# Kernel optimization log

Hardware: AMD Instinct MI355X
Metric: run time of the kernel (lower is better)

The kernel has to match this reference:

```python
import jax, jax.numpy as jnp
import numpy as np

B, NQ, K = 256, 16, 200           # batch, num_neg+1, num_keys
KEY_SIZE, QUERY_SIZE, HIDDEN = 64, 64, 128
NEG_INF_SCALE = -1000000000.0


def setup_inputs() -> dict:
    key = jax.random.key(0)
    ks = jax.random.split(key, 9)
    queries = jax.random.normal(ks[0], (B, NQ, QUERY_SIZE), dtype=jnp.float32)
    keys = jax.random.normal(ks[1], (B, K, KEY_SIZE), dtype=jnp.float32)
    cum_subs_masks = (jax.random.uniform(ks[2], (B, NQ, K, 1)) < 0.3).astype(jnp.float32)
    s = 1.0 / np.sqrt(HIDDEN)
    Wq = jax.random.normal(ks[3], (QUERY_SIZE, HIDDEN), dtype=jnp.float32) * s
    bq = jnp.zeros((HIDDEN,), dtype=jnp.float32)
    Wk = jax.random.normal(ks[4], (KEY_SIZE, HIDDEN), dtype=jnp.float32) * s
    bk = jnp.zeros((HIDDEN,), dtype=jnp.float32)
    Wv = jax.random.normal(ks[5], (HIDDEN, 1), dtype=jnp.float32) * s
    bv = jnp.zeros((1,), dtype=jnp.float32)
    return {"queries": queries, "keys": keys, "cum_subs_masks": cum_subs_masks,
            "num_neg": NQ - 1, "Wq": Wq, "bq": bq, "Wk": Wk, "bk": bk,
            "Wv": Wv, "bv": bv}


def reference(queries, keys, cum_subs_masks, num_neg, Wq, bq, Wk, bk, Wv, bv):
    # project once, broadcast instead of expanding keys per query (same math)
    qh = queries @ Wq + bq                 # (B, NQ, H)
    kh = keys @ Wk + bk                    # (B, K, H)
    h = jnp.tanh(qh[:, :, None, :] + kh[:, None, :, :])   # (B, NQ, K, H)
    scores = h @ Wv + bv                   # (B, NQ, K, 1)
    if cum_subs_masks is not None:
        scores = scores + cum_subs_masks * NEG_INF_SCALE
    attn_weight = jax.nn.softmax(scores, axis=-2)          # softmax over keys
    attn_out = jnp.sum(attn_weight * keys[:, None, :, :], axis=-2)  # (B, NQ, key_size)
    return (attn_out, attn_weight)
```

## Files before the change

kernel.cpp:

```cpp
#include <hip/hip_runtime.h>

namespace {

typedef __attribute__((ext_vector_type(8))) short short8;
typedef __attribute__((ext_vector_type(4))) float f32x4;

constexpr int kNB = 256;
constexpr int kNQ = 16;
constexpr int kNK = 200;
constexpr int kDK = 64;
constexpr int kNH = 128;
constexpr int kThreads = 1024;
constexpr int kS = 132;
constexpr float kNeg = -1000000000.0f;
constexpr float kC2 = 2.8853900817779268f;

constexpr int kKhFloats = kNK * kS;
constexpr int kScFloats = kNQ * kNK;
constexpr int kQhFloats = kNQ * kNH;
constexpr size_t kSmemBytes =
    (size_t)(kKhFloats + kScFloats + kQhFloats) * sizeof(float);

__device__ __forceinline__ float exp2_hw(float x) {
#if defined(__has_builtin)
# if __has_builtin(__builtin_amdgcn_exp2f)
  return __builtin_amdgcn_exp2f(x);
# else
  return __expf(x * 0.69314718055994531f);
# endif
#else
  return __expf(x * 0.69314718055994531f);
#endif
}

template <int CTRL>
__device__ __forceinline__ float dpp_add(float v) {
  int sw = __builtin_amdgcn_update_dpp(0, __float_as_int(v), CTRL, 0xF, 0xF, true);
  return v + __int_as_float(sw);
}

__device__ __forceinline__ short bf_hi(float x) {
  unsigned u = __float_as_uint(x);
  return (short)((u + 0x7FFFu + ((u >> 16) & 1u)) >> 16);
}
__device__ __forceinline__ float bf_f(short s) {
  return __uint_as_float(((unsigned)(unsigned short)s) << 16);
}
__device__ __forceinline__ void split8(float4 a, float4 b, short8& hi, short8& lo) {
  float v[8] = {a.x, a.y, a.z, a.w, b.x, b.y, b.z, b.w};
#pragma unroll
  for (int j = 0; j < 8; ++j) {
    const short h = bf_hi(v[j]);
    hi[j] = h;
    lo[j] = bf_hi(v[j] - bf_f(h));
  }
}

__launch_bounds__(kThreads)
__attribute__((amdgpu_waves_per_eu(4, 4)))
__global__ void bahdanau_fused(const float* __restrict__ queries,
                               const float* __restrict__ keys,
                               const float* __restrict__ masks,
                               const float* __restrict__ Wq,
                               const float* __restrict__ bq,
                               const float* __restrict__ Wk,
                               const float* __restrict__ bk,
                               const float* __restrict__ Wv,
                               float* __restrict__ out_attn,
                               float* __restrict__ out_w) {
  extern __shared__ __align__(16) float smem[];
  float* skh = smem;
  float* ssc = smem + kKhFloats;
  float* sqh = smem + kKhFloats + kScFloats;

  const int tid  = threadIdx.x;
  const int b    = blockIdx.x;
  const int lane = tid & 63;
  const int wave = __builtin_amdgcn_readfirstlane(tid >> 6);
  const int l15  = lane & 15;
  const int q16  = lane >> 4;
  const int hbase = 8 * l15;

  const float* kb = keys + (size_t)b * kNK * kDK;
  const float* qb = queries + (size_t)b * kNQ * kDK;

  {
    const int tc  = wave >> 1;
    const int odd = wave & 1;
    const int col = tc * 16 + l15;
    const int kj0 = q16 * 8;

    short8 bh[2], bl[2];
#pragma unroll
    for (int p = 0; p < 2; ++p) {
      float4 v0, v1;
      v0.x = Wk[(p * 32 + kj0 + 0) * kNH + col];
      v0.y = Wk[(p * 32 + kj0 + 1) * kNH + col];
      v0.z = Wk[(p * 32 + kj0 + 2) * kNH + col];
      v0.w = Wk[(p * 32 + kj0 + 3) * kNH + col];
      v1.x = Wk[(p * 32 + kj0 + 4) * kNH + col];
      v1.y = Wk[(p * 32 + kj0 + 5) * kNH + col];
      v1.z = Wk[(p * 32 + kj0 + 6) * kNH + col];
      v1.w = Wk[(p * 32 + kj0 + 7) * kNH + col];
      split8(v0, v1, bh[p], bl[p]);
    }
    const float bkc = bk[col];

    const int trB = odd ? 7 : 0;
    const int trE = odd ? 13 : 7;
    for (int tr = trB; tr < trE; ++tr) {
      f32x4 acc = {0.f, 0.f, 0.f, 0.f};
      const int row = tr * 16 + l15;
      const bool ok = row < kNK;
#pragma unroll
      for (int p = 0; p < 2; ++p) {
        float4 a0 = {0.f, 0.f, 0.f, 0.f}, a1 = {0.f, 0.f, 0.f, 0.f};
        if (ok) {
          const float* ap = kb + (size_t)row * kDK + p * 32 + kj0;
          a0 = *reinterpret_cast<const float4*>(ap);
          a1 = *reinterpret_cast<const float4*>(ap + 4);
        }
        short8 ah, al;
        split8(a0, a1, ah, al);
        acc = __builtin_amdgcn_mfma_f32_16x16x32_bf16(al, bh[p], acc, 0, 0, 0);
        acc = __builtin_amdgcn_mfma_f32_16x16x32_bf16(ah, bl[p], acc, 0, 0, 0);
        acc = __builtin_amdgcn_mfma_f32_16x16x32_bf16(ah, bh[p], acc, 0, 0, 0);
      }
#pragma unroll
      for (int r = 0; r < 4; ++r) {
        const int rr = tr * 16 + q16 * 4 + r;
        if (rr < kNK) skh[(size_t)rr * kS + col] = exp2_hw(kC2 * (acc[r] + bkc));
      }
    }

    if (odd) {
      short8 qbh[2], qbl[2];
#pragma unroll
      for (int p = 0; p < 2; ++p) {
        float4 v0, v1;
        v0.x = Wq[(p * 32 + kj0 + 0) * kNH + col];
        v0.y = Wq[(p * 32 + kj0 + 1) * kNH + col];
        v0.z = Wq[(p * 32 + kj0 + 2) * kNH + col];
        v0.w = Wq[(p * 32 + kj0 + 3) * kNH + col];
        v1.x = Wq[(p * 32 + kj0 + 4) * kNH + col];
        v1.y = Wq[(p * 32 + kj0 + 5) * kNH + col];
        v1.z = Wq[(p * 32 + kj0 + 6) * kNH + col];
        v1.w = Wq[(p * 32 + kj0 + 7) * kNH + col];
        split8(v0, v1, qbh[p], qbl[p]);
      }
      const float bqc = bq[col];
      f32x4 acc = {0.f, 0.f, 0.f, 0.f};
#pragma unroll
      for (int p = 0; p < 2; ++p) {
        const float* ap = qb + (size_t)l15 * kDK + p * 32 + kj0;
        const float4 a0 = *reinterpret_cast<const float4*>(ap);
        const float4 a1 = *reinterpret_cast<const float4*>(ap + 4);
        short8 ah, al;
        split8(a0, a1, ah, al);
        acc = __builtin_amdgcn_mfma_f32_16x16x32_bf16(al, qbh[p], acc, 0, 0, 0);
        acc = __builtin_amdgcn_mfma_f32_16x16x32_bf16(ah, qbl[p], acc, 0, 0, 0);
        acc = __builtin_amdgcn_mfma_f32_16x16x32_bf16(ah, qbh[p], acc, 0, 0, 0);
      }
#pragma unroll
      for (int r = 0; r < 4; ++r)
        sqh[(size_t)(q16 * 4 + r) * kNH + col] = exp2_hw(kC2 * (acc[r] + bqc));
    }
  }

  float wv2[8];
  {
    const float4 wva = *reinterpret_cast<const float4*>(&Wv[hbase]);
    const float4 wvb = *reinterpret_cast<const float4*>(&Wv[hbase + 4]);
    wv2[0] = -2.0f * wva.x; wv2[1] = -2.0f * wva.y;
    wv2[2] = -2.0f * wva.z; wv2[3] = -2.0f * wva.w;
    wv2[4] = -2.0f * wvb.x; wv2[5] = -2.0f * wvb.y;
    wv2[6] = -2.0f * wvb.z; wv2[7] = -2.0f * wvb.w;
  }

  __syncthreads();

  const int qg = wave >> 2;
  const int kg = wave & 3;
  float qreg[4][8];
#pragma unroll
  for (int qi = 0; qi < 4; ++qi) {
    const float4 qa  = *reinterpret_cast<const float4*>(&sqh[(4 * qg + qi) * kNH + hbase]);
    const float4 qb4 = *reinterpret_cast<const float4*>(&sqh[(4 * qg + qi) * kNH + hbase + 4]);
    qreg[qi][0] = qa.x;  qreg[qi][1] = qa.y;  qreg[qi][2] = qa.z;  qreg[qi][3] = qa.w;
    qreg[qi][4] = qb4.x; qreg[qi][5] = qb4.y; qreg[qi][6] = qb4.z; qreg[qi][7] = qb4.w;
  }
#pragma unroll
  for (int qi = 0; qi < 4; ++qi)
#pragma unroll
    for (int m = 0; m < 8; ++m) asm volatile("" : "+v"(qreg[qi][m]));

  {
    auto score_k = [&](int k) {
      const float* krow = &skh[(size_t)k * kS + hbase];
      const float4 ka  = *reinterpret_cast<const float4*>(krow);
      const float4 kb4 = *reinterpret_cast<const float4*>(krow + 4);
#pragma unroll
      for (int qi = 0; qi < 4; ++qi) {
        const float e0 = qreg[qi][0] * ka.x;
        const float e1 = qreg[qi][1] * ka.y;
        const float e2 = qreg[qi][2] * ka.z;
        const float e3 = qreg[qi][3] * ka.w;
        const float e4 = qreg[qi][4] * kb4.x;
        const float e5 = qreg[qi][5] * kb4.y;
        const float e6 = qreg[qi][6] * kb4.z;
        const float e7 = qreg[qi][7] * kb4.w;
        const float r0 = __builtin_amdgcn_rcpf(1.0f + e0);
        const float r1 = __builtin_amdgcn_rcpf(1.0f + e1);
        const float r2 = __builtin_amdgcn_rcpf(1.0f + e2);
        const float r3 = __builtin_amdgcn_rcpf(1.0f + e3);
        const float r4 = __builtin_amdgcn_rcpf(1.0f + e4);
        const float r5 = __builtin_amdgcn_rcpf(1.0f + e5);
        const float r6 = __builtin_amdgcn_rcpf(1.0f + e6);
        const float r7 = __builtin_amdgcn_rcpf(1.0f + e7);
        float acc0 = wv2[0] * r0;
        acc0 = fmaf(wv2[1], r1, acc0);
        acc0 = fmaf(wv2[2], r2, acc0);
        acc0 = fmaf(wv2[3], r3, acc0);
        float acc1 = wv2[4] * r4;
        acc1 = fmaf(wv2[5], r5, acc1);
        acc1 = fmaf(wv2[6], r6, acc1);
        acc1 = fmaf(wv2[7], r7, acc1);
        float acc = acc0 + acc1;
        acc = dpp_add<0xB1>(acc);
        acc = dpp_add<0x4E>(acc);
        acc = dpp_add<0x141>(acc);
        acc = dpp_add<0x140>(acc);
        if (l15 == 0) ssc[(4 * qg + qi) * kNK + k] = acc;
      }
    };
    for (int i = 0; i < 12; ++i) score_k(16 * i + 4 * kg + q16);
    if (kg < 2) score_k(192 + 4 * kg + q16);
  }

  const float* mrow = masks + ((size_t)b * kNQ + wave) * kNK;
  const bool tail = lane < (kNK - 192);
  const float mm0 = mrow[lane];
  const float mm1 = mrow[lane + 64];
  const float mm2 = mrow[lane + 128];
  const float mm3 = tail ? mrow[lane + 192] : 0.0f;

  __syncthreads();

  {
    const float* sr = &ssc[wave * kNK];
    float v0 = fmaf(mm0, kNeg, sr[lane]);
    float v1 = fmaf(mm1, kNeg, sr[lane + 64]);
    float v2 = fmaf(mm2, kNeg, sr[lane + 128]);
    float v3 = tail ? fmaf(mm3, kNeg, sr[lane + 192]) : -1e30f;
    float m = fmaxf(fmaxf(v0, v1), fmaxf(v2, v3));
#pragma unroll
    for (int off = 32; off > 0; off >>= 1) m = fmaxf(m, __shfl_xor(m, off, 64));
    const float e0 = __expf(v0 - m);
    const float e1 = __expf(v1 - m);
    const float e2 = __expf(v2 - m);
    const float e3 = tail ? __expf(v3 - m) : 0.f;
    float sum = (e0 + e1) + (e2 + e3);
#pragma unroll
    for (int off = 32; off > 0; off >>= 1) sum += __shfl_xor(sum, off, 64);
    const float rs = __builtin_amdgcn_rcpf(sum);
    float* og = out_w + ((size_t)b * kNQ + wave) * kNK;
    float* sw = &ssc[wave * kNK];
    const float w0 = e0 * rs, w1 = e1 * rs, w2 = e2 * rs, w3 = e3 * rs;
    sw[lane]       = w0;  og[lane]       = w0;
    sw[lane + 64]  = w1;  og[lane + 64]  = w1;
    sw[lane + 128] = w2;  og[lane + 128] = w2;
    if (tail) { sw[lane + 192] = w3; og[lane + 192] = w3; }
  }
  __syncthreads();

  {
    float* pk = skh;
    const int kstart = 52 * kg;
    const int kend = (kg == 3) ? kNK : (kstart + 52);
    const float* kb2 = kb + lane;
    float acc[4] = {0.f, 0.f, 0.f, 0.f};
    for (int k0 = kstart; k0 < kend; k0 += 4) {
      const float kv0 = kb2[(size_t)(k0 + 0) * kDK];
      const float kv1 = kb2[(size_t)(k0 + 1) * kDK];
      const float kv2 = kb2[(size_t)(k0 + 2) * kDK];
      const float kv3 = kb2[(size_t)(k0 + 3) * kDK];
#pragma unroll
      for (int qi = 0; qi < 4; ++qi) {
        const float4 wq = *reinterpret_cast<const float4*>(&ssc[(4 * qg + qi) * kNK + k0]);
        acc[qi] = fmaf(wq.x, kv0, acc[qi]);
        acc[qi] = fmaf(wq.y, kv1, acc[qi]);
        acc[qi] = fmaf(wq.z, kv2, acc[qi]);
        acc[qi] = fmaf(wq.w, kv3, acc[qi]);
      }
    }
#pragma unroll
    for (int qi = 0; qi < 4; ++qi)
      pk[((4 * qg + qi) * 4 + kg) * kDK + lane] = acc[qi];
  }
  __syncthreads();

  {
    const float* pk = skh;
    const float r = pk[(wave * 4 + 0) * kDK + lane] + pk[(wave * 4 + 1) * kDK + lane] +
                    pk[(wave * 4 + 2) * kDK + lane] + pk[(wave * 4 + 3) * kDK + lane];
    out_attn[((size_t)b * kNQ + wave) * kDK + lane] = r;
  }
}

}

extern "C" void kernel_launch(void* const* d_in, const int* in_sizes, int n_in,
                              void* d_out, int out_size, void* d_ws, size_t ws_size,
                              hipStream_t stream) {
  const float* queries = (const float*)d_in[0];
  const float* keys    = (const float*)d_in[1];
  const float* masks   = (const float*)d_in[2];
  const float* Wq = (const float*)d_in[4];
  const float* bq = (const float*)d_in[5];
  const float* Wk = (const float*)d_in[6];
  const float* bk = (const float*)d_in[7];
  const float* Wv = (const float*)d_in[8];

  float* out_attn = (float*)d_out;
  float* out_w    = out_attn + (size_t)kNB * kNQ * kDK;

  hipFuncSetAttribute((const void*)bahdanau_fused,
                      hipFuncAttributeMaxDynamicSharedMemorySize, (int)kSmemBytes);

  bahdanau_fused<<<kNB, kThreads, kSmemBytes, stream>>>(queries, keys, masks, Wq, bq,
                                                        Wk, bk, Wv, out_attn, out_w);
}
```

Before: 38.40 us.

## Split fused kernel into hidden-half score kernel plus softmax/GEMV kernel

Splits the single fused per-batch kernel into two launches. The first computes projections and partial tanh scores for half of the hidden dimension per block, giving 512 blocks with smaller shared memory, and writes partial scores to workspace. The second sums the two partials, applies mask and softmax, and does the weighted key sum. The aim is more parallelism and occupancy than 256 large blocks offer, at the cost of an extra launch, a workspace round trip, and recomputing the query projection in both halves. It falls back to the fused kernel if the workspace is too small.

Measured after the change: 45.87 us. +19.4%, slower.

```diff
diff --git a/kernel.cpp b/kernel.cpp
--- a/kernel.cpp
+++ b/kernel.cpp
@@ -10,16 +10,11 @@
 constexpr int kNK = 200;
 constexpr int kDK = 64;
 constexpr int kNH = 128;
-constexpr int kThreads = 1024;
-constexpr int kS = 132;
 constexpr float kNeg = -1000000000.0f;
 constexpr float kC2 = 2.8853900817779268f;
 
-constexpr int kKhFloats = kNK * kS;
-constexpr int kScFloats = kNQ * kNK;
-constexpr int kQhFloats = kNQ * kNH;
-constexpr size_t kSmemBytes =
-    (size_t)(kKhFloats + kScFloats + kQhFloats) * sizeof(float);
+constexpr int kS1 = 66;
+constexpr size_t kWsNeed = (size_t)kNB * 2 * kNQ * kNK * sizeof(float);
 
 __device__ __forceinline__ float exp2_hw(float x) {
 #if defined(__has_builtin)
@@ -55,6 +50,252 @@
     lo[j] = bf_hi(v[j] - bf_f(h));
   }
 }
+
+__launch_bounds__(512)
+__attribute__((amdgpu_waves_per_eu(4, 4)))
+__global__ void proj_score(const float* __restrict__ queries,
+                           const float* __restrict__ keys,
+                           const float* __restrict__ Wq,
+                           const float* __restrict__ bq,
+                           const float* __restrict__ Wk,
+                           const float* __restrict__ bk,
+                           const float* __restrict__ Wv,
+                           float* __restrict__ ps) {
+  __shared__ float skh[kNK * kS1];
+  __shared__ float sqh[kNQ * kS1];
+
+  const int tid  = threadIdx.x;
+  const int b    = blockIdx.x >> 1;
+  const int hb   = blockIdx.x & 1;
+  const int lane = tid & 63;
+  const int wave = __builtin_amdgcn_readfirstlane(tid >> 6);
+  const int l15  = lane & 15;
+  const int q16  = lane >> 4;
+
+  const float* kb = keys + (size_t)b * kNK * kDK;
+  const float* qb = queries + (size_t)b * kNQ * kDK;
+
+  {
+    const int tc   = wave >> 1;
+    const int odd  = wave & 1;
+    const int lcol = tc * 16 + l15;
+    const int gcol = hb * 64 + lcol;
+    const int kj0  = q16 * 8;
+
+    short8 bh[2], bl[2];
+#pragma unroll
+    for (int p = 0; p < 2; ++p) {
+      float4 v0, v1;
+      v0.x = Wk[(p * 32 + kj0 + 0) * kNH + gcol];
+      v0.y = Wk[(p * 32 + kj0 + 1) * kNH + gcol];
+      v0.z = Wk[(p * 32 + kj0 + 2) * kNH + gcol];
+      v0.w = Wk[(p * 32 + kj0 + 3) * kNH + gcol];
+      v1.x = Wk[(p * 32 + kj0 + 4) * kNH + gcol];
+      v1.y = Wk[(p * 32 + kj0 + 5) * kNH + gcol];
+      v1.z = Wk[(p * 32 + kj0 + 6) * kNH + gcol];
+      v1.w = Wk[(p * 32 + kj0 + 7) * kNH + gcol];
+      split8(v0, v1, bh[p], bl[p]);
+    }
+    const float bkc = bk[gcol];
+
+    const int trB = odd ? 7 : 0;
+    const int trE = odd ? 13 : 7;
+    for (int tr = trB; tr < trE; ++tr) {
+      f32x4 acc = {0.f, 0.f, 0.f, 0.f};
+      const int row = tr * 16 + l15;
+      const bool ok = row < kNK;
+#pragma unroll
+      for (int p = 0; p < 2; ++p) {
+        float4 a0 = {0.f, 0.f, 0.f, 0.f}, a1 = {0.f, 0.f, 0.f, 0.f};
+        if (ok) {
+          const float* ap = kb + (size_t)row * kDK + p * 32 + kj0;
+          a0 = *reinterpret_cast<const float4*>(ap);
+          a1 = *reinterpret_cast<const float4*>(ap + 4);
+        }
+        short8 ah, al;
+        split8(a0, a1, ah, al);
+        acc = __builtin_amdgcn_mfma_f32_16x16x32_bf16(al, bh[p], acc, 0, 0, 0);
+        acc = __builtin_amdgcn_mfma_f32_16x16x32_bf16(ah, bl[p], acc, 0, 0, 0);
+        acc = __builtin_amdgcn_mfma_f32_16x16x32_bf16(ah, bh[p], acc, 0, 0, 0);
+      }
+#pragma unroll
+      for (int r = 0; r < 4; ++r) {
+        const int rr = tr * 16 + q16 * 4 + r;
+        if (rr < kNK) skh[rr * kS1 + lcol] = exp2_hw(kC2 * (acc[r] + bkc));
+      }
+    }
+
+    if (odd) {
+      short8 qbh[2], qbl[2];
+#pragma unroll
+      for (int p = 0; p < 2; ++p) {
+        float4 v0, v1;
+        v0.x = Wq[(p * 32 + kj0 + 0) * kNH + gcol];
+        v0.y = Wq[(p * 32 + kj0 + 1) * kNH + gcol];
+        v0.z = Wq[(p * 32 + kj0 + 2) * kNH + gcol];
+        v0.w = Wq[(p * 32 + kj0 + 3) * kNH + gcol];
+        v1.x = Wq[(p * 32 + kj0 + 4) * kNH + gcol];
+        v1.y = Wq[(p * 32 + kj0 + 5) * kNH + gcol];
+        v1.z = Wq[(p * 32 + kj0 + 6) * kNH + gcol];
+        v1.w = Wq[(p * 32 + kj0 + 7) * kNH + gcol];
+        split8(v0, v1, qbh[p], qbl[p]);
+      }
+      const float bqc = bq[gcol];
+      f32x4 acc = {0.f, 0.f, 0.f, 0.f};
+#pragma unroll
+      for (int p = 0; p < 2; ++p) {
+        const float* ap = qb + (size_t)l15 * kDK + p * 32 + kj0;
+        const float4 a0 = *reinterpret_cast<const float4*>(ap);
+        const float4 a1 = *reinterpret_cast<const float4*>(ap + 4);
+        short8 ah, al;
+        split8(a0, a1, ah, al);
+        acc = __builtin_amdgcn_mfma_f32_16x16x32_bf16(al, qbh[p], acc, 0, 0, 0);
+        acc = __builtin_amdgcn_mfma_f32_16x16x32_bf16(ah, qbl[p], acc, 0, 0, 0);
+        acc = __builtin_amdgcn_mfma_f32_16x16x32_bf16(ah, qbh[p], acc, 0, 0, 0);
+      }
+#pragma unroll
+      for (int r = 0; r < 4; ++r)
+        sqh[(q16 * 4 + r) * kS1 + lcol] = exp2_hw(kC2 * (acc[r] + bqc));
+    }
+  }
+
+  float wv2[4];
+  {
+    const float4 w4 = *reinterpret_cast<const float4*>(&Wv[hb * 64 + 4 * l15]);
+    wv2[0] = -2.0f * w4.x; wv2[1] = -2.0f * w4.y;
+    wv2[2] = -2.0f * w4.z; wv2[3] = -2.0f * w4.w;
+  }
+
+  __syncthreads();
+
+  const int qg = wave >> 1;
+  const int kg = wave & 1;
+  float qreg[4][4];
+#pragma unroll
+  for (int qi = 0; qi < 4; ++qi) {
+    const float4 q4 = *reinterpret_cast<const float4*>(&sqh[(4 * qg + qi) * kS1 + 4 * l15]);
+    qreg[qi][0] = q4.x; qreg[qi][1] = q4.y; qreg[qi][2] = q4.z; qreg[qi][3] = q4.w;
+  }
+#pragma unroll
+  for (int qi = 0; qi < 4; ++qi)
+#pragma unroll
+    for (int m = 0; m < 4; ++m) asm volatile("" : "+v"(qreg[qi][m]));
+
+  float* pw = ps + ((size_t)(b * 2 + hb) * kNQ) * kNK;
+  for (int i = 0; i < 25; ++i) {
+    const int k = 8 * i + 4 * kg + q16;
+    const float4 ek = *reinterpret_cast<const float4*>(&skh[k * kS1 + 4 * l15]);
+#pragma unroll
+    for (int qi = 0; qi < 4; ++qi) {
+      const float e0 = qreg[qi][0] * ek.x;
+      const float e1 = qreg[qi][1] * ek.y;
+      const float e2 = qreg[qi][2] * ek.z;
+      const float e3 = qreg[qi][3] * ek.w;
+      const float r0 = __builtin_amdgcn_rcpf(1.0f + e0);
+      const float r1 = __builtin_amdgcn_rcpf(1.0f + e1);
+      const float r2 = __builtin_amdgcn_rcpf(1.0f + e2);
+      const float r3 = __builtin_amdgcn_rcpf(1.0f + e3);
+      float acc = wv2[0] * r0;
+      acc = fmaf(wv2[1], r1, acc);
+      acc = fmaf(wv2[2], r2, acc);
+      acc = fmaf(wv2[3], r3, acc);
+      acc = dpp_add<0xB1>(acc);
+      acc = dpp_add<0x4E>(acc);
+      acc = dpp_add<0x141>(acc);
+      acc = dpp_add<0x140>(acc);
+      if (l15 == 0) pw[(4 * qg + qi) * kNK + k] = acc;
+    }
+  }
+}
+
+__launch_bounds__(1024)
+__global__ void softmax_gemv(const float* __restrict__ keys,
+                             const float* __restrict__ masks,
+                             const float* __restrict__ ps,
+                             float* __restrict__ out_attn,
+                             float* __restrict__ out_w) {
+  __shared__ float sw[kNQ * kNK];
+  __shared__ float pk[kNQ * 4 * kDK];
+
+  const int tid  = threadIdx.x;
+  const int b    = blockIdx.x;
+  const int lane = tid & 63;
+  const int wave = __builtin_amdgcn_readfirstlane(tid >> 6);
+
+  const float* kb = keys + (size_t)b * kNK * kDK;
+
+  {
+    const float* p0 = ps + ((size_t)(b * 2 + 0) * kNQ + wave) * kNK;
+    const float* p1 = ps + ((size_t)(b * 2 + 1) * kNQ + wave) * kNK;
+    const float* mrow = masks + ((size_t)b * kNQ + wave) * kNK;
+    const bool tail = lane < (kNK - 192);
+    float v0 = fmaf(mrow[lane],       kNeg, p0[lane]       + p1[lane]);
+    float v1 = fmaf(mrow[lane + 64],  kNeg, p0[lane + 64]  + p1[lane + 64]);
+    float v2 = fmaf(mrow[lane + 128], kNeg, p0[lane + 128] + p1[lane + 128]);
+    float v3 = tail ? fmaf(mrow[lane + 192], kNeg, p0[lane + 192] + p1[lane + 192])
+                    : -1e30f;
+    float m = fmaxf(fmaxf(v0, v1), fmaxf(v2, v3));
+#pragma unroll
+    for (int off = 32; off > 0; off >>= 1) m = fmaxf(m, __shfl_xor(m, off, 64));
+    const float e0 = __expf(v0 - m);
+    const float e1 = __expf(v1 - m);
+    const float e2 = __expf(v2 - m);
+    const float e3 = tail ? __expf(v3 - m) : 0.f;
+    float sum = (e0 + e1) + (e2 + e3);
+#pragma unroll
+    for (int off = 32; off > 0; off >>= 1) sum += __shfl_xor(sum, off, 64);
+    const float rs = __builtin_amdgcn_rcpf(sum);
+    float* og = out_w + ((size_t)b * kNQ + wave) * kNK;
+    float* swr = &sw[wave * kNK];
+    const float w0 = e0 * rs, w1 = e1 * rs, w2 = e2 * rs, w3 = e3 * rs;
+    swr[lane]       = w0;  og[lane]       = w0;
+    swr[lane + 64]  = w1;  og[lane + 64]  = w1;
+    swr[lane + 128] = w2;  og[lane + 128] = w2;
+    if (tail) { swr[lane + 192] = w3; og[lane + 192] = w3; }
+  }
+  __syncthreads();
+
+  {
+    const int qg = wave >> 2;
+    const int kg = wave & 3;
+    const int kstart = 52 * kg;
+    const int kend = (kg == 3) ? kNK : (kstart + 52);
+    const float* kb2 = kb + lane;
+    float acc[4] = {0.f, 0.f, 0.f, 0.f};
+    for (int k0 = kstart; k0 < kend; k0 += 4) {
+      const float kv0 = kb2[(size_t)(k0 + 0) * kDK];
+      const float kv1 = kb2[(size_t)(k0 + 1) * kDK];
+      const float kv2 = kb2[(size_t)(k0 + 2) * kDK];
+      const float kv3 = kb2[(size_t)(k0 + 3) * kDK];
+#pragma unroll
+      for (int qi = 0; qi < 4; ++qi) {
+        const float4 wq = *reinterpret_cast<const float4*>(&sw[(4 * qg + qi) * kNK + k0]);
+        acc[qi] = fmaf(wq.x, kv0, acc[qi]);
+        acc[qi] = fmaf(wq.y, kv1, acc[qi]);
+        acc[qi] = fmaf(wq.z, kv2, acc[qi]);
+        acc[qi] = fmaf(wq.w, kv3, acc[qi]);
+      }
+    }
+#pragma unroll
+    for (int qi = 0; qi < 4; ++qi)
+      pk[((4 * qg + qi) * 4 + kg) * kDK + lane] = acc[qi];
+  }
+  __syncthreads();
+
+  {
+    const float r = pk[(wave * 4 + 0) * kDK + lane] + pk[(wave * 4 + 1) * kDK + lane] +
+                    pk[(wave * 4 + 2) * kDK + lane] + pk[(wave * 4 + 3) * kDK + lane];
+    out_attn[((size_t)b * kNQ + wave) * kDK + lane] = r;
+  }
+}
+
+constexpr int kThreads = 1024;
+constexpr int kS = 132;
+constexpr int kKhFloats = kNK * kS;
+constexpr int kScFloats = kNQ * kNK;
+constexpr int kQhFloats = kNQ * kNH;
+constexpr size_t kSmemBytes =
+    (size_t)(kKhFloats + kScFloats + kQhFloats) * sizeof(float);
 
 __launch_bounds__(kThreads)
 __attribute__((amdgpu_waves_per_eu(4, 4)))
@@ -105,7 +346,6 @@
       split8(v0, v1, bh[p], bl[p]);
     }
     const float bkc = bk[col];
-
     const int trB = odd ? 7 : 0;
     const int trE = odd ? 13 : 7;
     for (int tr = trB; tr < trE; ++tr) {
@@ -132,7 +372,6 @@
         if (rr < kNK) skh[(size_t)rr * kS + col] = exp2_hw(kC2 * (acc[r] + bkc));
       }
     }
-
     if (odd) {
       short8 qbh[2], qbl[2];
 #pragma unroll
@@ -189,10 +428,6 @@
     qreg[qi][0] = qa.x;  qreg[qi][1] = qa.y;  qreg[qi][2] = qa.z;  qreg[qi][3] = qa.w;
     qreg[qi][4] = qb4.x; qreg[qi][5] = qb4.y; qreg[qi][6] = qb4.z; qreg[qi][7] = qb4.w;
   }
-#pragma unroll
-  for (int qi = 0; qi < 4; ++qi)
-#pragma unroll
-    for (int m = 0; m < 8; ++m) asm volatile("" : "+v"(qreg[qi][m]));
 
   {
     auto score_k = [&](int k) {
@@ -264,12 +499,12 @@
     for (int off = 32; off > 0; off >>= 1) sum += __shfl_xor(sum, off, 64);
     const float rs = __builtin_amdgcn_rcpf(sum);
     float* og = out_w + ((size_t)b * kNQ + wave) * kNK;
-    float* sw = &ssc[wave * kNK];
+    float* swr = &ssc[wave * kNK];
     const float w0 = e0 * rs, w1 = e1 * rs, w2 = e2 * rs, w3 = e3 * rs;
-    sw[lane]       = w0;  og[lane]       = w0;
-    sw[lane + 64]  = w1;  og[lane + 64]  = w1;
-    sw[lane + 128] = w2;  og[lane + 128] = w2;
-    if (tail) { sw[lane + 192] = w3; og[lane + 192] = w3; }
+    swr[lane]       = w0;  og[lane]       = w0;
+    swr[lane + 64]  = w1;  og[lane + 64]  = w1;
+    swr[lane + 128] = w2;  og[lane + 128] = w2;
+    if (tail) { swr[lane + 192] = w3; og[lane + 192] = w3; }
   }
   __syncthreads();
 
@@ -324,9 +559,14 @@
   float* out_attn = (float*)d_out;
   float* out_w    = out_attn + (size_t)kNB * kNQ * kDK;
 
-  hipFuncSetAttribute((const void*)bahdanau_fused,
-                      hipFuncAttributeMaxDynamicSharedMemorySize, (int)kSmemBytes);
-
-  bahdanau_fused<<<kNB, kThreads, kSmemBytes, stream>>>(queries, keys, masks, Wq, bq,
-                                                        Wk, bk, Wv, out_attn, out_w);
-}
+  if (ws_size >= kWsNeed) {
+    float* ps = (float*)d_ws;
+    proj_score<<<kNB * 2, 512, 0, stream>>>(queries, keys, Wq, bq, Wk, bk, Wv, ps);
+    softmax_gemv<<<kNB, 1024, 0, stream>>>(keys, masks, ps, out_attn, out_w);
+  } else {
+    hipFuncSetAttribute((const void*)bahdanau_fused,
+                        hipFuncAttributeMaxDynamicSharedMemorySize, (int)kSmemBytes);
+    bahdanau_fused<<<kNB, kThreads, kSmemBytes, stream>>>(queries, keys, masks, Wq, bq,
+                                                          Wk, bk, Wv, out_attn, out_w);
+  }
+}
```

## Halve block to 8 waves and redistribute projection, score and softmax work

Applied to the files above, without the earlier changes.

The block shrinks from 16 to 8 waves, and each stage's work split is redone. Every wave now computes one 16-column slice of both the query and key projections. The score loop is split into 2 key groups instead of 4 and prefetches the next key row from shared memory. Each wave also handles two softmax rows, and the weighted sum reduces 2 partials instead of 4. The bf16 split uses the library conversions and the tanh argument is fused into an fma. The aim is to cut barrier and wave overhead and raise per-wave ILP, at the cost of less parallelism per block.

Result: slower. 39.20 us (+2.1%).

```diff
diff --git a/kernel.cpp b/kernel.cpp
--- a/kernel.cpp
+++ b/kernel.cpp
@@ -1,4 +1,5 @@
 #include <hip/hip_runtime.h>
+#include <hip/hip_bf16.h>
 
 namespace {
 
@@ -10,7 +11,7 @@
 constexpr int kNK = 200;
 constexpr int kDK = 64;
 constexpr int kNH = 128;
-constexpr int kThreads = 1024;
+constexpr int kThreads = 512;
 constexpr int kS = 132;
 constexpr float kNeg = -1000000000.0f;
 constexpr float kC2 = 2.8853900817779268f;
@@ -39,35 +40,29 @@
   return v + __int_as_float(sw);
 }
 
-__device__ __forceinline__ short bf_hi(float x) {
-  unsigned u = __float_as_uint(x);
-  return (short)((u + 0x7FFFu + ((u >> 16) & 1u)) >> 16);
-}
-__device__ __forceinline__ float bf_f(short s) {
-  return __uint_as_float(((unsigned)(unsigned short)s) << 16);
-}
 __device__ __forceinline__ void split8(float4 a, float4 b, short8& hi, short8& lo) {
   float v[8] = {a.x, a.y, a.z, a.w, b.x, b.y, b.z, b.w};
 #pragma unroll
   for (int j = 0; j < 8; ++j) {
-    const short h = bf_hi(v[j]);
-    hi[j] = h;
-    lo[j] = bf_hi(v[j] - bf_f(h));
+    const __hip_bfloat16 h = __float2bfloat16(v[j]);
+    hi[j] = (short)__bfloat16_as_ushort(h);
+    const __hip_bfloat16 l = __float2bfloat16(v[j] - __bfloat162float(h));
+    lo[j] = (short)__bfloat16_as_ushort(l);
   }
 }
 
 __launch_bounds__(kThreads)
-__attribute__((amdgpu_waves_per_eu(4, 4)))
-__global__ void bahdanau_fused(const float* __restrict__ queries,
-                               const float* __restrict__ keys,
-                               const float* __restrict__ masks,
-                               const float* __restrict__ Wq,
-                               const float* __restrict__ bq,
-                               const float* __restrict__ Wk,
-                               const float* __restrict__ bk,
-                               const float* __restrict__ Wv,
-                               float* __restrict__ out_attn,
-                               float* __restrict__ out_w) {
+__attribute__((amdgpu_waves_per_eu(2, 2)))
+__global__ void bahdanau_fused8(const float* __restrict__ queries,
+                                const float* __restrict__ keys,
+                                const float* __restrict__ masks,
+                                const float* __restrict__ Wq,
+                                const float* __restrict__ bq,
+                                const float* __restrict__ Wk,
+                                const float* __restrict__ bk,
+                                const float* __restrict__ Wv,
+                                float* __restrict__ out_attn,
+                                float* __restrict__ out_w) {
   extern __shared__ __align__(16) float smem[];
   float* skh = smem;
   float* ssc = smem + kKhFloats;
@@ -85,12 +80,43 @@
   const float* qb = queries + (size_t)b * kNQ * kDK;
 
   {
-    const int tc  = wave >> 1;
-    const int odd = wave & 1;
-    const int col = tc * 16 + l15;
+    const int col = wave * 16 + l15;
     const int kj0 = q16 * 8;
 
-    short8 bh[2], bl[2];
+    short8 fh[2], fl[2];
+
+#pragma unroll
+    for (int p = 0; p < 2; ++p) {
+      float4 v0, v1;
+      v0.x = Wq[(p * 32 + kj0 + 0) * kNH + col];
+      v0.y = Wq[(p * 32 + kj0 + 1) * kNH + col];
+      v0.z = Wq[(p * 32 + kj0 + 2) * kNH + col];
+      v0.w = Wq[(p * 32 + kj0 + 3) * kNH + col];
+      v1.x = Wq[(p * 32 + kj0 + 4) * kNH + col];
+      v1.y = Wq[(p * 32 + kj0 + 5) * kNH + col];
+      v1.z = Wq[(p * 32 + kj0 + 6) * kNH + col];
+      v1.w = Wq[(p * 32 + kj0 + 7) * kNH + col];
+      split8(v0, v1, fh[p], fl[p]);
+    }
+    {
+      const float bqc = bq[col];
+      f32x4 acc = {0.f, 0.f, 0.f, 0.f};
+#pragma unroll
+      for (int p = 0; p < 2; ++p) {
+        const float* ap = qb + (size_t)l15 * kDK + p * 32 + kj0;
+        const float4 a0 = *reinterpret_cast<const float4*>(ap);
+        const float4 a1 = *reinterpret_cast<const float4*>(ap + 4);
+        short8 ah, al;
+        split8(a0, a1, ah, al);
+        acc = __builtin_amdgcn_mfma_f32_16x16x32_bf16(al, fh[p], acc, 0, 0, 0);
+        acc = __builtin_amdgcn_mfma_f32_16x16x32_bf16(ah, fl[p], acc, 0, 0, 0);
+        acc = __builtin_amdgcn_mfma_f32_16x16x32_bf16(ah, fh[p], acc, 0, 0, 0);
+      }
+#pragma unroll
+      for (int r = 0; r < 4; ++r)
+        sqh[(size_t)(q16 * 4 + r) * kNH + col] = exp2_hw(kC2 * (acc[r] + bqc));
+    }
+
 #pragma unroll
     for (int p = 0; p < 2; ++p) {
       float4 v0, v1;
@@ -102,13 +128,10 @@
       v1.y = Wk[(p * 32 + kj0 + 5) * kNH + col];
       v1.z = Wk[(p * 32 + kj0 + 6) * kNH + col];
       v1.w = Wk[(p * 32 + kj0 + 7) * kNH + col];
-      split8(v0, v1, bh[p], bl[p]);
+      split8(v0, v1, fh[p], fl[p]);
     }
     const float bkc = bk[col];
-
-    const int trB = odd ? 7 : 0;
-    const int trE = odd ? 13 : 7;
-    for (int tr = trB; tr < trE; ++tr) {
+    for (int tr = 0; tr < 13; ++tr) {
       f32x4 acc = {0.f, 0.f, 0.f, 0.f};
       const int row = tr * 16 + l15;
       const bool ok = row < kNK;
@@ -122,48 +145,15 @@
         }
         short8 ah, al;
         split8(a0, a1, ah, al);
-        acc = __builtin_amdgcn_mfma_f32_16x16x32_bf16(al, bh[p], acc, 0, 0, 0);
-        acc = __builtin_amdgcn_mfma_f32_16x16x32_bf16(ah, bl[p], acc, 0, 0, 0);
-        acc = __builtin_amdgcn_mfma_f32_16x16x32_bf16(ah, bh[p], acc, 0, 0, 0);
+        acc = __builtin_amdgcn_mfma_f32_16x16x32_bf16(al, fh[p], acc, 0, 0, 0);
+        acc = __builtin_amdgcn_mfma_f32_16x16x32_bf16(ah, fl[p], acc, 0, 0, 0);
+        acc = __builtin_amdgcn_mfma_f32_16x16x32_bf16(ah, fh[p], acc, 0, 0, 0);
       }
 #pragma unroll
       for (int r = 0; r < 4; ++r) {
         const int rr = tr * 16 + q16 * 4 + r;
         if (rr < kNK) skh[(size_t)rr * kS + col] = exp2_hw(kC2 * (acc[r] + bkc));
       }
-    }
-
-    if (odd) {
-      short8 qbh[2], qbl[2];
-#pragma unroll
-      for (int p = 0; p < 2; ++p) {
-        float4 v0, v1;
-        v0.x = Wq[(p * 32 + kj0 + 0) * kNH + col];
-        v0.y = Wq[(p * 32 + kj0 + 1) * kNH + col];
-        v0.z = Wq[(p * 32 + kj0 + 2) * kNH + col];
-        v0.w = Wq[(p * 32 + kj0 + 3) * kNH + col];
-        v1.x = Wq[(p * 32 + kj0 + 4) * kNH + col];
-        v1.y = Wq[(p * 32 + kj0 + 5) * kNH + col];
-        v1.z = Wq[(p * 32 + kj0 + 6) * kNH + col];
-        v1.w = Wq[(p * 32 + kj0 + 7) * kNH + col];
-        split8(v0, v1, qbh[p], qbl[p]);
-      }
-      const float bqc = bq[col];
-      f32x4 acc = {0.f, 0.f, 0.f, 0.f};
-#pragma unroll
-      for (int p = 0; p < 2; ++p) {
-        const float* ap = qb + (size_t)l15 * kDK + p * 32 + kj0;
-        const float4 a0 = *reinterpret_cast<const float4*>(ap);
-        const float4 a1 = *reinterpret_cast<const float4*>(ap + 4);
-        short8 ah, al;
-        split8(a0, a1, ah, al);
-        acc = __builtin_amdgcn_mfma_f32_16x16x32_bf16(al, qbh[p], acc, 0, 0, 0);
-        acc = __builtin_amdgcn_mfma_f32_16x16x32_bf16(ah, qbl[p], acc, 0, 0, 0);
-        acc = __builtin_amdgcn_mfma_f32_16x16x32_bf16(ah, qbh[p], acc, 0, 0, 0);
-      }
-#pragma unroll
-      for (int r = 0; r < 4; ++r)
-        sqh[(size_t)(q16 * 4 + r) * kNH + col] = exp2_hw(kC2 * (acc[r] + bqc));
     }
   }
 
@@ -179,8 +169,8 @@
 
   __syncthreads();
 
-  const int qg = wave >> 2;
-  const int kg = wave & 3;
+  const int qg = wave >> 1;
+  const int kg = wave & 1;
   float qreg[4][8];
 #pragma unroll
   for (int qi = 0; qi < 4; ++qi) {
@@ -189,34 +179,29 @@
     qreg[qi][0] = qa.x;  qreg[qi][1] = qa.y;  qreg[qi][2] = qa.z;  qreg[qi][3] = qa.w;
     qreg[qi][4] = qb4.x; qreg[qi][5] = qb4.y; qreg[qi][6] = qb4.z; qreg[qi][7] = qb4.w;
   }
-#pragma unroll
-  for (int qi = 0; qi < 4; ++qi)
-#pragma unroll
-    for (int m = 0; m < 8; ++m) asm volatile("" : "+v"(qreg[qi][m]));
-
-  {
-    auto score_k = [&](int k) {
-      const float* krow = &skh[(size_t)k * kS + hbase];
-      const float4 ka  = *reinterpret_cast<const float4*>(krow);
-      const float4 kb4 = *reinterpret_cast<const float4*>(krow + 4);
+
+  {
+    const float* kl = &skh[(size_t)(4 * kg + q16) * kS + hbase];
+    float4 ka  = *reinterpret_cast<const float4*>(kl);
+    float4 kb4 = *reinterpret_cast<const float4*>(kl + 4);
+    for (int i = 0; i < 25; ++i) {
+      float4 na = ka, nb = kb4;
+      if (i < 24) {
+        const float* nx = kl + (size_t)(i + 1) * 8 * kS;
+        na = *reinterpret_cast<const float4*>(nx);
+        nb = *reinterpret_cast<const float4*>(nx + 4);
+      }
+      const int k = 8 * i + 4 * kg + q16;
 #pragma unroll
       for (int qi = 0; qi < 4; ++qi) {
-        const float e0 = qreg[qi][0] * ka.x;
-        const float e1 = qreg[qi][1] * ka.y;
-        const float e2 = qreg[qi][2] * ka.z;
-        const float e3 = qreg[qi][3] * ka.w;
-        const float e4 = qreg[qi][4] * kb4.x;
-        const float e5 = qreg[qi][5] * kb4.y;
-        const float e6 = qreg[qi][6] * kb4.z;
-        const float e7 = qreg[qi][7] * kb4.w;
-        const float r0 = __builtin_amdgcn_rcpf(1.0f + e0);
-        const float r1 = __builtin_amdgcn_rcpf(1.0f + e1);
-        const float r2 = __builtin_amdgcn_rcpf(1.0f + e2);
-        const float r3 = __builtin_amdgcn_rcpf(1.0f + e3);
-        const float r4 = __builtin_amdgcn_rcpf(1.0f + e4);
-        const float r5 = __builtin_amdgcn_rcpf(1.0f + e5);
-        const float r6 = __builtin_amdgcn_rcpf(1.0f + e6);
-        const float r7 = __builtin_amdgcn_rcpf(1.0f + e7);
+        const float r0 = __builtin_amdgcn_rcpf(fmaf(qreg[qi][0], ka.x, 1.0f));
+        const float r1 = __builtin_amdgcn_rcpf(fmaf(qreg[qi][1], ka.y, 1.0f));
+        const float r2 = __builtin_amdgcn_rcpf(fmaf(qreg[qi][2], ka.z, 1.0f));
+        const float r3 = __builtin_amdgcn_rcpf(fmaf(qreg[qi][3], ka.w, 1.0f));
+        const float r4 = __builtin_amdgcn_rcpf(fmaf(qreg[qi][4], kb4.x, 1.0f));
+        const float r5 = __builtin_amdgcn_rcpf(fmaf(qreg[qi][5], kb4.y, 1.0f));
+        const float r6 = __builtin_amdgcn_rcpf(fmaf(qreg[qi][6], kb4.z, 1.0f));
+        const float r7 = __builtin_amdgcn_rcpf(fmaf(qreg[qi][7], kb4.w, 1.0f));
         float acc0 = wv2[0] * r0;
         acc0 = fmaf(wv2[1], r1, acc0);
         acc0 = fmaf(wv2[2], r2, acc0);
@@ -232,26 +217,32 @@
         acc = dpp_add<0x140>(acc);
         if (l15 == 0) ssc[(4 * qg + qi) * kNK + k] = acc;
       }
-    };
-    for (int i = 0; i < 12; ++i) score_k(16 * i + 4 * kg + q16);
-    if (kg < 2) score_k(192 + 4 * kg + q16);
-  }
-
-  const float* mrow = masks + ((size_t)b * kNQ + wave) * kNK;
+      ka = na; kb4 = nb;
+    }
+  }
+
   const bool tail = lane < (kNK - 192);
-  const float mm0 = mrow[lane];
-  const float mm1 = mrow[lane + 64];
-  const float mm2 = mrow[lane + 128];
-  const float mm3 = tail ? mrow[lane + 192] : 0.0f;
+  float mm[2][4];
+#pragma unroll
+  for (int rp = 0; rp < 2; ++rp) {
+    const int q = wave + 8 * rp;
+    const float* mrow = masks + ((size_t)b * kNQ + q) * kNK;
+    mm[rp][0] = mrow[lane];
+    mm[rp][1] = mrow[lane + 64];
+    mm[rp][2] = mrow[lane + 128];
+    mm[rp][3] = tail ? mrow[lane + 192] : 0.0f;
+  }
 
   __syncthreads();
 
-  {
-    const float* sr = &ssc[wave * kNK];
-    float v0 = fmaf(mm0, kNeg, sr[lane]);
-    float v1 = fmaf(mm1, kNeg, sr[lane + 64]);
-    float v2 = fmaf(mm2, kNeg, sr[lane + 128]);
-    float v3 = tail ? fmaf(mm3, kNeg, sr[lane + 192]) : -1e30f;
+#pragma unroll
+  for (int rp = 0; rp < 2; ++rp) {
+    const int q = wave + 8 * rp;
+    const float* sr = &ssc[q * kNK];
+    float v0 = fmaf(mm[rp][0], kNeg, sr[lane]);
+    float v1 = fmaf(mm[rp][1], kNeg, sr[lane + 64]);
+    float v2 = fmaf(mm[rp][2], kNeg, sr[lane + 128]);
+    float v3 = tail ? fmaf(mm[rp][3], kNeg, sr[lane + 192]) : -1e30f;
     float m = fmaxf(fmaxf(v0, v1), fmaxf(v2, v3));
 #pragma unroll
     for (int off = 32; off > 0; off >>= 1) m = fmaxf(m, __shfl_xor(m, off, 64));
@@ -263,23 +254,22 @@
 #pragma unroll
     for (int off = 32; off > 0; off >>= 1) sum += __shfl_xor(sum, off, 64);
     const float rs = __builtin_amdgcn_rcpf(sum);
-    float* og = out_w + ((size_t)b * kNQ + wave) * kNK;
-    float* sw = &ssc[wave * kNK];
+    float* og = out_w + ((size_t)b * kNQ + q) * kNK;
+    float* swr = &ssc[q * kNK];
     const float w0 = e0 * rs, w1 = e1 * rs, w2 = e2 * rs, w3 = e3 * rs;
-    sw[lane]       = w0;  og[lane]       = w0;
-    sw[lane + 64]  = w1;  og[lane + 64]  = w1;
-    sw[lane + 128] = w2;  og[lane + 128] = w2;
-    if (tail) { sw[lane + 192] = w3; og[lane + 192] = w3; }
+    swr[lane]       = w0;  og[lane]       = w0;
+    swr[lane + 64]  = w1;  og[lane + 64]  = w1;
+    swr[lane + 128] = w2;  og[lane + 128] = w2;
+    if (tail) { swr[lane + 192] = w3; og[lane + 192] = w3; }
   }
   __syncthreads();
 
   {
     float* pk = skh;
-    const int kstart = 52 * kg;
-    const int kend = (kg == 3) ? kNK : (kstart + 52);
+    const int kstart = 100 * kg;
     const float* kb2 = kb + lane;
     float acc[4] = {0.f, 0.f, 0.f, 0.f};
-    for (int k0 = kstart; k0 < kend; k0 += 4) {
+    for (int k0 = kstart; k0 < kstart + 100; k0 += 4) {
       const float kv0 = kb2[(size_t)(k0 + 0) * kDK];
       const float kv1 = kb2[(size_t)(k0 + 1) * kDK];
       const float kv2 = kb2[(size_t)(k0 + 2) * kDK];
@@ -295,15 +285,18 @@
     }
 #pragma unroll
     for (int qi = 0; qi < 4; ++qi)
-      pk[((4 * qg + qi) * 4 + kg) * kDK + lane] = acc[qi];
+      pk[((4 * qg + qi) * 2 + kg) * kDK + lane] = acc[qi];
   }
   __syncthreads();
 
   {
     const float* pk = skh;
-    const float r = pk[(wave * 4 + 0) * kDK + lane] + pk[(wave * 4 + 1) * kDK + lane] +
-                    pk[(wave * 4 + 2) * kDK + lane] + pk[(wave * 4 + 3) * kDK + lane];
-    out_attn[((size_t)b * kNQ + wave) * kDK + lane] = r;
+#pragma unroll
+    for (int rp = 0; rp < 2; ++rp) {
+      const int q = wave + 8 * rp;
+      const float r = pk[(q * 2 + 0) * kDK + lane] + pk[(q * 2 + 1) * kDK + lane];
+      out_attn[((size_t)b * kNQ + q) * kDK + lane] = r;
+    }
   }
 }
 
@@ -324,9 +317,8 @@
   float* out_attn = (float*)d_out;
   float* out_w    = out_attn + (size_t)kNB * kNQ * kDK;
 
-  hipFuncSetAttribute((const void*)bahdanau_fused,
+  hipFuncSetAttribute((const void*)bahdanau_fused8,
                       hipFuncAttributeMaxDynamicSharedMemorySize, (int)kSmemBytes);
-
-  bahdanau_fused<<<kNB, kThreads, kSmemBytes, stream>>>(queries, keys, masks, Wq, bq,
-                                                        Wk, bk, Wv, out_attn, out_w);
-}
+  bahdanau_fused8<<<kNB, kThreads, kSmemBytes, stream>>>(queries, keys, masks, Wq, bq,
+                                                         Wk, bk, Wv, out_attn, out_w);
+}
```
